# Performance work log

Hardware: AMD Instinct MI355X
Metric: run time of the kernel (lower is better)

The kernel has to match this reference:

```python
import jax, jax.numpy as jnp
import numpy as np

DIM = 1024
DEPTH = 7
PAR = 8
N_NODES = 2 ** (DEPTH + 1) - 1  # 255
WIDTH = PAR * N_NODES  # 2040


def setup_inputs() -> dict:
    key = jax.random.key(0)
    k1, k2, k3, k4 = jax.random.split(key, 4)
    init_k = float(np.sqrt(1.0 / DIM))
    init_k2 = float(np.sqrt(1.0 / ((DEPTH + 1) * PAR)))
    oldx = jax.random.normal(k1, (4, 2048, DIM), dtype=jnp.float32)
    W_in = jax.random.uniform(k2, (WIDTH, DIM), jnp.float32, -init_k, init_k)
    b_in = jax.random.uniform(k3, (WIDTH,), jnp.float32, -init_k, init_k)
    W_out = jax.random.uniform(k4, (DIM, WIDTH), jnp.float32, -init_k2, init_k2)
    return {"oldx": oldx, "W_in": W_in, "b_in": b_in, "W_out": W_out}


def reference(oldx, W_in, b_in, W_out):
    x = oldx.reshape(-1, DIM)                      # [B, dim]
    B = x.shape[0]
    logits = x @ W_in.T + b_in                     # [B, width] dense GEMM over ALL nodes
    decisions = (logits > 0).astype(jnp.int32).reshape(B, PAR, N_NODES)
    acts = jax.nn.silu(logits).reshape(B, PAR, N_NODES)

    # Tree traversal: mark root, then descend DEPTH levels by each node's sign bit.
    current = jnp.zeros((B, PAR), dtype=jnp.int32)
    dmap = jax.nn.one_hot(current, N_NODES, dtype=acts.dtype)  # root node marked
    for d in range(DEPTH):
        cur_platform = 2 ** d - 1
        next_platform = 2 ** (d + 1) - 1
        moves = jnp.take_along_axis(decisions, current[..., None], axis=2)[..., 0]
        current = (current - cur_platform) * 2 + moves + next_platform
        dmap = dmap + jax.nn.one_hot(current, N_NODES, dtype=acts.dtype)

    masked = acts * jax.lax.stop_gradient(dmap)    # only depth+1 nodes per tree survive
    out = masked.reshape(B, WIDTH) @ W_out.T       # [B, dim]
    return out.reshape(oldx.shape)
```

## Files before the change

kernel.cpp:

```cpp
#include <hip/hip_runtime.h>
#include <math.h>

#define DIM 1024
#define DEPTH 7
#define PAR 8
#define N_NODES 255
#define WIDTH 2040
#define MARGIN 0.01f

#define REPLANE(p) ((((p) & 1) << 3) | ((((p) >> 1) & 1) << 4) | ((((p) >> 2) & 1) << 5))

#define PIN4(u) asm volatile("" : "+v"((u).x), "+v"((u).y), "+v"((u).z), "+v"((u).w))

typedef _Float16 half2v __attribute__((ext_vector_type(2)));

__device__ __forceinline__ half2v as_h2(unsigned int u) {
    union { unsigned int u; half2v h; } c; c.u = u; return c.h;
}
__device__ __forceinline__ unsigned int pack_h2(float a, float b) {
    union { half2v h; unsigned int u; } c;
    c.h = (half2v){(_Float16)a, (_Float16)b};
    return c.u;
}

__device__ __forceinline__ float dot2h(unsigned int a, unsigned int b, float c) {
#if __has_builtin(__builtin_amdgcn_fdot2)
    return __builtin_amdgcn_fdot2(as_h2(a), as_h2(b), c, false);
#else
    half2v ha = as_h2(a), hb = as_h2(b);
    c = fmaf((float)ha.x, (float)hb.x, c);
    return fmaf((float)ha.y, (float)hb.y, c);
#endif
}

__device__ __forceinline__ float foldK(float a, float b, int K) {
    const bool hi = (threadIdx.x & (unsigned)K) != 0;
    const float keep = hi ? b : a;
    const float send = hi ? a : b;
    return keep + __shfl_xor(send, K, 64);
}

#define TRANS_BLOCKS 512

__global__ __launch_bounds__(256) void prep_kernel(
    const float* __restrict__ W_out,
    const float* __restrict__ W_in,
    unsigned short* __restrict__ WoT,
    unsigned int* __restrict__ Wh)
{
    __shared__ float tile[64][65];
    if (blockIdx.x < TRANS_BLOCKS) {
        const int w0 = (int)(blockIdx.x & 31) * 64;
        const int d0 = (int)(blockIdx.x >> 5) * 64;
        const int tid = (int)threadIdx.x;
        const int sub = tid & 15;
        const int grp = tid >> 4;

        #pragma unroll
        for (int pass = 0; pass < 4; ++pass) {
            const int dl = pass * 16 + grp;
            const int wl = sub * 4;
            const int w = w0 + wl;
            const int d = d0 + dl;
            float4 v = make_float4(0.f, 0.f, 0.f, 0.f);
            if (w + 3 < WIDTH) {
                v = *(const float4*)(W_out + (size_t)d * WIDTH + w);
            } else {
                float t0 = (w + 0 < WIDTH) ? W_out[(size_t)d * WIDTH + w + 0] : 0.f;
                float t1 = (w + 1 < WIDTH) ? W_out[(size_t)d * WIDTH + w + 1] : 0.f;
                float t2 = (w + 2 < WIDTH) ? W_out[(size_t)d * WIDTH + w + 2] : 0.f;
                float t3 = (w + 3 < WIDTH) ? W_out[(size_t)d * WIDTH + w + 3] : 0.f;
                v = make_float4(t0, t1, t2, t3);
            }
            tile[dl][wl + 0] = v.x; tile[dl][wl + 1] = v.y;
            tile[dl][wl + 2] = v.z; tile[dl][wl + 3] = v.w;
        }
        __syncthreads();
        #pragma unroll
        for (int pass = 0; pass < 4; ++pass) {
            const int wl = pass * 16 + grp;
            const int dl = sub * 4;
            const int w = w0 + wl;
            if (w < WIDTH) {
                uint2 pk;
                pk.x = pack_h2(tile[dl + 0][wl], tile[dl + 1][wl]);
                pk.y = pack_h2(tile[dl + 2][wl], tile[dl + 3][wl]);
                *(uint2*)(WoT + (size_t)w * DIM + d0 + dl) = pk;
            }
        }
    } else {
        const int n4 = WIDTH * DIM / 4;
        const int nthr = ((int)gridDim.x - TRANS_BLOCKS) * 256;
        for (int i = ((int)blockIdx.x - TRANS_BLOCKS) * 256 + (int)threadIdx.x;
             i < n4; i += nthr) {
            float4 v = ((const float4*)W_in)[i];
            uint2 pk;
            pk.x = pack_h2(v.x, v.y);
            pk.y = pack_h2(v.z, v.w);
            ((uint2*)Wh)[i] = pk;
        }
    }
}

__global__ __launch_bounds__(256) void fff_f16_kernel(
    const float* __restrict__ x,
    const float* __restrict__ W_in,
    const float* __restrict__ b_in,
    const unsigned int* __restrict__ Wh,
    const unsigned short* __restrict__ WoT,
    float* __restrict__ out,
    int B)
{
    const int wave = (int)((blockIdx.x * blockDim.x + threadIdx.x) >> 6);
    const int lane = (int)(threadIdx.x & 63);
    if (wave >= B) return;

    const float* xr = x + (size_t)wave * DIM;
    unsigned int xp[8];
    {
        float4 a0 = *(const float4*)(xr + lane * 8 + 0);
        float4 a1 = *(const float4*)(xr + lane * 8 + 4);
        float4 a2 = *(const float4*)(xr + 512 + lane * 8 + 0);
        float4 a3 = *(const float4*)(xr + 512 + lane * 8 + 4);
        xp[0] = pack_h2(a0.x, a0.y);
        xp[1] = pack_h2(a0.z, a0.w);
        xp[2] = pack_h2(a1.x, a1.y);
        xp[3] = pack_h2(a1.z, a1.w);
        xp[4] = pack_h2(a2.x, a2.y);
        xp[5] = pack_h2(a2.z, a2.w);
        xp[6] = pack_h2(a3.x, a3.y);
        xp[7] = pack_h2(a3.z, a3.w);
    }

    float acc[16];
    #pragma unroll
    for (int i = 0; i < 16; ++i) acc[i] = 0.f;

    unsigned long long nodes = 0ULL;
    const int myp = ((lane >> 3) & 1) | (((lane >> 4) & 1) << 1) | (((lane >> 5) & 1) << 2);

    #pragma unroll 1
    for (int d = 0; d <= DEPTH; ++d) {
        int gidx[PAR];
        #pragma unroll
        for (int p = 0; p < PAR; ++p) {
            const int np = (int)((nodes >> (8 * p)) & 0xffULL);
            gidx[p] = p * N_NODES + np;
        }

        const int ga = (lane & 8) ? gidx[1] : gidx[0];
        const int gb = (lane & 8) ? gidx[3] : gidx[2];
        const int gc = (lane & 8) ? gidx[5] : gidx[4];
        const int gd = (lane & 8) ? gidx[7] : gidx[6];
        const int ge = (lane & 16) ? gb : ga;
        const int gf = (lane & 16) ? gd : gc;
        const int gmine = (lane & 32) ? gf : ge;
        const float bias = b_in[gmine];

        uint4 wv0[PAR], wv1[PAR];
        #pragma unroll
        for (int p = 0; p < PAR; ++p) {
            const unsigned short* wo = WoT + (size_t)gidx[p] * DIM;
            wv0[p] = *(const uint4*)(wo + lane * 8);
            wv1[p] = *(const uint4*)(wo + 512 + lane * 8);
        }
        __builtin_amdgcn_sched_barrier(0);

        float partial[PAR];
        #pragma unroll
        for (int p = 0; p < PAR; ++p) {
            const unsigned int* wr = Wh + (size_t)gidx[p] * (DIM / 2);
            const uint4 u0 = *(const uint4*)(wr + lane * 4);
            const uint4 u1 = *(const uint4*)(wr + 256 + lane * 4);
            float s = 0.f;
            s = dot2h(xp[0], u0.x, s);
            s = dot2h(xp[1], u0.y, s);
            s = dot2h(xp[2], u0.z, s);
            s = dot2h(xp[3], u0.w, s);
            s = dot2h(xp[4], u1.x, s);
            s = dot2h(xp[5], u1.y, s);
            s = dot2h(xp[6], u1.z, s);
            s = dot2h(xp[7], u1.w, s);
            partial[p] = s;
        }

        const float c01 = foldK(partial[0], partial[1], 8);
        const float c23 = foldK(partial[2], partial[3], 8);
        const float c45 = foldK(partial[4], partial[5], 8);
        const float c67 = foldK(partial[6], partial[7], 8);
        const float d0f = foldK(c01, c23, 16);
        const float d1f = foldK(c45, c67, 16);
        float e = foldK(d0f, d1f, 32);
        e += __shfl_xor(e, 1, 64);
        e += __shfl_xor(e, 2, 64);
        e += __shfl_xor(e, 4, 64);
        float my = e + bias;

        if (d < DEPTH) {
            const unsigned long long bal = __ballot(fabsf(my) < MARGIN);
            unsigned rm = 0;
            #pragma unroll
            for (int p = 0; p < PAR; ++p)
                rm |= ((unsigned)((bal >> REPLANE(p)) & 1ULL)) << p;
            if (rm) {
                while (rm) {
                    const int p = __builtin_ctz(rm); rm &= (rm - 1u);
                    const int np = (int)((nodes >> (8 * p)) & 0xffULL);
                    const int gi = p * N_NODES + np;
                    const float* wr = W_in + (size_t)gi * DIM;
                    float s = 0.f;
                    #pragma unroll
                    for (int q = 0; q < 4; ++q) {
                        const int off = (q & 1) * 4 + (q >> 1) * 512 + lane * 8;
                        const float4 fx = *(const float4*)(xr + off);
                        const float4 fw = *(const float4*)(wr + off);
                        s = fmaf(fx.x, fw.x, s); s = fmaf(fx.y, fw.y, s);
                        s = fmaf(fx.z, fw.z, s); s = fmaf(fx.w, fw.w, s);
                    }
                    #pragma unroll
                    for (int off = 32; off >= 1; off >>= 1)
                        s += __shfl_xor(s, off, 64);
                    const float lf = s + b_in[gi];
                    my = (myp == p) ? lf : my;
                }
            }
        }

        const float act_mine = my / (1.0f + __expf(-my));
        const unsigned long long pos = __ballot(my > 0.0f);

        float act[PAR];
        #pragma unroll
        for (int p = 0; p < PAR; ++p)
            act[p] = __shfl(act_mine, REPLANE(p), 64);

        #pragma unroll
        for (int p = 0; p < PAR; ++p) { PIN4(wv0[p]); PIN4(wv1[p]); }

        #pragma unroll
        for (int p = 0; p < PAR; ++p) {
            const float a_ = act[p];
            half2v h_;
            h_ = as_h2(wv0[p].x); acc[0]  = fmaf((float)h_.x, a_, acc[0]);  acc[1]  = fmaf((float)h_.y, a_, acc[1]);
            h_ = as_h2(wv0[p].y); acc[2]  = fmaf((float)h_.x, a_, acc[2]);  acc[3]  = fmaf((float)h_.y, a_, acc[3]);
            h_ = as_h2(wv0[p].z); acc[4]  = fmaf((float)h_.x, a_, acc[4]);  acc[5]  = fmaf((float)h_.y, a_, acc[5]);
            h_ = as_h2(wv0[p].w); acc[6]  = fmaf((float)h_.x, a_, acc[6]);  acc[7]  = fmaf((float)h_.y, a_, acc[7]);
            h_ = as_h2(wv1[p].x); acc[8]  = fmaf((float)h_.x, a_, acc[8]);  acc[9]  = fmaf((float)h_.y, a_, acc[9]);
            h_ = as_h2(wv1[p].y); acc[10] = fmaf((float)h_.x, a_, acc[10]); acc[11] = fmaf((float)h_.y, a_, acc[11]);
            h_ = as_h2(wv1[p].z); acc[12] = fmaf((float)h_.x, a_, acc[12]); acc[13] = fmaf((float)h_.y, a_, acc[13]);
            h_ = as_h2(wv1[p].w); acc[14] = fmaf((float)h_.x, a_, acc[14]); acc[15] = fmaf((float)h_.y, a_, acc[15]);
        }

        if (d < DEPTH) {
            #pragma unroll
            for (int p = 0; p < PAR; ++p) {
                const int np = (int)((nodes >> (8 * p)) & 0xffULL);
                const unsigned long long nn = (unsigned long long)
                    (2 * np + 1 + (int)((pos >> REPLANE(p)) & 1ULL));
                nodes = (nodes & ~(0xffULL << (8 * p))) | (nn << (8 * p));
            }
        }
    }

    float* orow = out + (size_t)wave * DIM;
    *(float4*)(orow + lane * 8 + 0)       = make_float4(acc[0],  acc[1],  acc[2],  acc[3]);
    *(float4*)(orow + lane * 8 + 4)       = make_float4(acc[4],  acc[5],  acc[6],  acc[7]);
    *(float4*)(orow + 512 + lane * 8 + 0) = make_float4(acc[8],  acc[9],  acc[10], acc[11]);
    *(float4*)(orow + 512 + lane * 8 + 4) = make_float4(acc[12], acc[13], acc[14], acc[15]);
}

__global__ __launch_bounds__(256) void fff_fallback_kernel(
    const float* __restrict__ x, const float* __restrict__ W_in,
    const float* __restrict__ b_in, const float* __restrict__ W_out,
    float* __restrict__ out, int B)
{
    const int wave = (int)((blockIdx.x * blockDim.x + threadIdx.x) >> 6);
    const int lane = (int)(threadIdx.x & 63);
    if (wave >= B) return;

    const float* xr = x + (size_t)wave * DIM;
    float4 x4[4];
    x4[0] = *(const float4*)(xr + lane * 8 + 0);
    x4[1] = *(const float4*)(xr + lane * 8 + 4);
    x4[2] = *(const float4*)(xr + 512 + lane * 8 + 0);
    x4[3] = *(const float4*)(xr + 512 + lane * 8 + 4);

    float acc[16];
    #pragma unroll
    for (int i = 0; i < 16; ++i) acc[i] = 0.f;
    int node[PAR];
    #pragma unroll
    for (int p = 0; p < PAR; ++p) node[p] = 0;

    for (int d = 0; d <= DEPTH; ++d) {
        #pragma unroll
        for (int p = 0; p < PAR; ++p) {
            const int gidx = p * N_NODES + node[p];
            const float* wr = W_in + (size_t)gidx * DIM;
            const float4 wa = *(const float4*)(wr + lane * 8 + 0);
            const float4 wb = *(const float4*)(wr + lane * 8 + 4);
            const float4 wc = *(const float4*)(wr + 512 + lane * 8 + 0);
            const float4 wd = *(const float4*)(wr + 512 + lane * 8 + 4);
            float s = 0.f;
            s = fmaf(x4[0].x, wa.x, s); s = fmaf(x4[0].y, wa.y, s);
            s = fmaf(x4[0].z, wa.z, s); s = fmaf(x4[0].w, wa.w, s);
            s = fmaf(x4[1].x, wb.x, s); s = fmaf(x4[1].y, wb.y, s);
            s = fmaf(x4[1].z, wb.z, s); s = fmaf(x4[1].w, wb.w, s);
            s = fmaf(x4[2].x, wc.x, s); s = fmaf(x4[2].y, wc.y, s);
            s = fmaf(x4[2].z, wc.z, s); s = fmaf(x4[2].w, wc.w, s);
            s = fmaf(x4[3].x, wd.x, s); s = fmaf(x4[3].y, wd.y, s);
            s = fmaf(x4[3].z, wd.z, s); s = fmaf(x4[3].w, wd.w, s);
            #pragma unroll
            for (int off = 32; off >= 1; off >>= 1)
                s += __shfl_xor(s, off, 64);
            const float logit = s + b_in[gidx];
            const float act = logit / (1.0f + __expf(-logit));
            #pragma unroll
            for (int k = 0; k < 2; ++k) {
                #pragma unroll
                for (int j = 0; j < 8; ++j) {
                    const int e = k * 512 + lane * 8 + j;
                    acc[k * 8 + j] = fmaf(act, W_out[(size_t)e * WIDTH + gidx], acc[k * 8 + j]);
                }
            }
            node[p] = 2 * node[p] + 1 + ((logit > 0.0f) ? 1 : 0);
        }
    }

    float* orow = out + (size_t)wave * DIM;
    *(float4*)(orow + lane * 8 + 0)       = make_float4(acc[0],  acc[1],  acc[2],  acc[3]);
    *(float4*)(orow + lane * 8 + 4)       = make_float4(acc[4],  acc[5],  acc[6],  acc[7]);
    *(float4*)(orow + 512 + lane * 8 + 0) = make_float4(acc[8],  acc[9],  acc[10], acc[11]);
    *(float4*)(orow + 512 + lane * 8 + 4) = make_float4(acc[12], acc[13], acc[14], acc[15]);
}

extern "C" void kernel_launch(void* const* d_in, const int* in_sizes, int n_in,
                              void* d_out, int out_size, void* d_ws, size_t ws_size,
                              hipStream_t stream) {
    const float* oldx  = (const float*)d_in[0];
    const float* W_in  = (const float*)d_in[1];
    const float* b_in  = (const float*)d_in[2];
    const float* W_out = (const float*)d_in[3];
    float* out = (float*)d_out;

    const int B = in_sizes[0] / DIM;

    const size_t half = (size_t)WIDTH * DIM * sizeof(unsigned short);
    const bool use_lp = (ws_size >= 2 * half) && (d_ws != nullptr);

    const int blocks = (B + 3) / 4;

    if (use_lp) {
        unsigned short* WoT = (unsigned short*)d_ws;
        unsigned int*   Wh  = (unsigned int*)((char*)d_ws + half);
        prep_kernel<<<TRANS_BLOCKS + 1024, 256, 0, stream>>>(W_out, W_in, WoT, Wh);
        fff_f16_kernel<<<blocks, 256, 0, stream>>>(oldx, W_in, b_in, Wh, WoT, out, B);
    } else {
        fff_fallback_kernel<<<blocks, 256, 0, stream>>>(oldx, W_in, b_in, W_out, out, B);
    }
}
```

Baseline: 187.1 us.

## Split tree traversal and output accumulation into two kernels via workspace

Splits the fused kernel in two. Stage 1 does the tree traversal and writes per-row activations and node indices to workspace. Stage 2 gathers the fp16 W_out rows and accumulates the output, so each kernel has lower register pressure and stage 1 no longer keeps 16 prefetched W_out vectors live. The cost is an extra kernel launch, a global round trip for the activations and indices, and losing the overlap of W_out loads with the traversal. The split path is used when the workspace is large enough; otherwise the original fused kernel, now without prefetch, runs.

```diff
diff --git a/kernel.cpp b/kernel.cpp
--- a/kernel.cpp
+++ b/kernel.cpp
@@ -9,8 +9,6 @@
 #define MARGIN 0.01f
 
 #define REPLANE(p) ((((p) & 1) << 3) | ((((p) >> 1) & 1) << 4) | ((((p) >> 2) & 1) << 5))
-
-#define PIN4(u) asm volatile("" : "+v"((u).x), "+v"((u).y), "+v"((u).z), "+v"((u).w))
 
 typedef _Float16 half2v __attribute__((ext_vector_type(2)));
 
@@ -102,13 +100,13 @@
     }
 }
 
-__global__ __launch_bounds__(256) void fff_f16_kernel(
+__global__ __launch_bounds__(256) void fff_stage1_kernel(
     const float* __restrict__ x,
     const float* __restrict__ W_in,
     const float* __restrict__ b_in,
     const unsigned int* __restrict__ Wh,
-    const unsigned short* __restrict__ WoT,
-    float* __restrict__ out,
+    float* __restrict__ acts,
+    unsigned short* __restrict__ gidx_out,
     int B)
 {
     const int wave = (int)((blockIdx.x * blockDim.x + threadIdx.x) >> 6);
@@ -132,10 +130,6 @@
         xp[7] = pack_h2(a3.z, a3.w);
     }
 
-    float acc[16];
-    #pragma unroll
-    for (int i = 0; i < 16; ++i) acc[i] = 0.f;
-
     unsigned long long nodes = 0ULL;
     const int myp = ((lane >> 3) & 1) | (((lane >> 4) & 1) << 1) | (((lane >> 5) & 1) << 2);
 
@@ -156,15 +150,6 @@
         const int gf = (lane & 16) ? gd : gc;
         const int gmine = (lane & 32) ? gf : ge;
         const float bias = b_in[gmine];
-
-        uint4 wv0[PAR], wv1[PAR];
-        #pragma unroll
-        for (int p = 0; p < PAR; ++p) {
-            const unsigned short* wo = WoT + (size_t)gidx[p] * DIM;
-            wv0[p] = *(const uint4*)(wo + lane * 8);
-            wv1[p] = *(const uint4*)(wo + 512 + lane * 8);
-        }
-        __builtin_amdgcn_sched_barrier(0);
 
         float partial[PAR];
         #pragma unroll
@@ -229,31 +214,208 @@
         const float act_mine = my / (1.0f + __expf(-my));
         const unsigned long long pos = __ballot(my > 0.0f);
 
-        float act[PAR];
-        #pragma unroll
-        for (int p = 0; p < PAR; ++p)
-            act[p] = __shfl(act_mine, REPLANE(p), 64);
-
-        #pragma unroll
-        for (int p = 0; p < PAR; ++p) { PIN4(wv0[p]); PIN4(wv1[p]); }
-
-        #pragma unroll
-        for (int p = 0; p < PAR; ++p) {
-            const float a_ = act[p];
-            half2v h_;
-            h_ = as_h2(wv0[p].x); acc[0]  = fmaf((float)h_.x, a_, acc[0]);  acc[1]  = fmaf((float)h_.y, a_, acc[1]);
-            h_ = as_h2(wv0[p].y); acc[2]  = fmaf((float)h_.x, a_, acc[2]);  acc[3]  = fmaf((float)h_.y, a_, acc[3]);
-            h_ = as_h2(wv0[p].z); acc[4]  = fmaf((float)h_.x, a_, acc[4]);  acc[5]  = fmaf((float)h_.y, a_, acc[5]);
-            h_ = as_h2(wv0[p].w); acc[6]  = fmaf((float)h_.x, a_, acc[6]);  acc[7]  = fmaf((float)h_.y, a_, acc[7]);
-            h_ = as_h2(wv1[p].x); acc[8]  = fmaf((float)h_.x, a_, acc[8]);  acc[9]  = fmaf((float)h_.y, a_, acc[9]);
-            h_ = as_h2(wv1[p].y); acc[10] = fmaf((float)h_.x, a_, acc[10]); acc[11] = fmaf((float)h_.y, a_, acc[11]);
-            h_ = as_h2(wv1[p].z); acc[12] = fmaf((float)h_.x, a_, acc[12]); acc[13] = fmaf((float)h_.y, a_, acc[13]);
-            h_ = as_h2(wv1[p].w); acc[14] = fmaf((float)h_.x, a_, acc[14]); acc[15] = fmaf((float)h_.y, a_, acc[15]);
+        if ((lane & 7) == 0) {
+            const int slot = (wave << 6) + (d << 3) + myp;
+            acts[slot] = act_mine;
+            gidx_out[slot] = (unsigned short)gmine;
         }
 
         if (d < DEPTH) {
             #pragma unroll
             for (int p = 0; p < PAR; ++p) {
+                const int np = (int)((nodes >> (8 * p)) & 0xffULL);
+                const unsigned long long nn = (unsigned long long)
+                    (2 * np + 1 + (int)((pos >> REPLANE(p)) & 1ULL));
+                nodes = (nodes & ~(0xffULL << (8 * p))) | (nn << (8 * p));
+            }
+        }
+    }
+}
+
+__global__ __launch_bounds__(256) void fff_stage2_kernel(
+    const float* __restrict__ acts,
+    const unsigned short* __restrict__ gidx16,
+    const unsigned short* __restrict__ WoT,
+    float* __restrict__ out,
+    int B)
+{
+    const int wave = (int)((blockIdx.x * blockDim.x + threadIdx.x) >> 6);
+    const int lane = (int)(threadIdx.x & 63);
+    if (wave >= B) return;
+
+    const int base = wave << 6;
+    const float a_l = acts[base + lane];
+    const int   g_l = (int)gidx16[base + lane];
+
+    float acc[16];
+    #pragma unroll
+    for (int i = 0; i < 16; ++i) acc[i] = 0.f;
+
+    #pragma unroll 4
+    for (int e = 0; e < 64; ++e) {
+        const float a_ = __shfl(a_l, e, 64);
+        const int   g  = __shfl(g_l, e, 64);
+        const unsigned short* wo = WoT + (size_t)g * DIM;
+        const uint4 u0 = *(const uint4*)(wo + lane * 8);
+        const uint4 u1 = *(const uint4*)(wo + 512 + lane * 8);
+        half2v h_;
+        h_ = as_h2(u0.x); acc[0]  = fmaf((float)h_.x, a_, acc[0]);  acc[1]  = fmaf((float)h_.y, a_, acc[1]);
+        h_ = as_h2(u0.y); acc[2]  = fmaf((float)h_.x, a_, acc[2]);  acc[3]  = fmaf((float)h_.y, a_, acc[3]);
+        h_ = as_h2(u0.z); acc[4]  = fmaf((float)h_.x, a_, acc[4]);  acc[5]  = fmaf((float)h_.y, a_, acc[5]);
+        h_ = as_h2(u0.w); acc[6]  = fmaf((float)h_.x, a_, acc[6]);  acc[7]  = fmaf((float)h_.y, a_, acc[7]);
+        h_ = as_h2(u1.x); acc[8]  = fmaf((float)h_.x, a_, acc[8]);  acc[9]  = fmaf((float)h_.y, a_, acc[9]);
+        h_ = as_h2(u1.y); acc[10] = fmaf((float)h_.x, a_, acc[10]); acc[11] = fmaf((float)h_.y, a_, acc[11]);
+        h_ = as_h2(u1.z); acc[12] = fmaf((float)h_.x, a_, acc[12]); acc[13] = fmaf((float)h_.y, a_, acc[13]);
+        h_ = as_h2(u1.w); acc[14] = fmaf((float)h_.x, a_, acc[14]); acc[15] = fmaf((float)h_.y, a_, acc[15]);
+    }
+
+    float* orow = out + (size_t)wave * DIM;
+    *(float4*)(orow + lane * 8 + 0)       = make_float4(acc[0],  acc[1],  acc[2],  acc[3]);
+    *(float4*)(orow + lane * 8 + 4)       = make_float4(acc[4],  acc[5],  acc[6],  acc[7]);
+    *(float4*)(orow + 512 + lane * 8 + 0) = make_float4(acc[8],  acc[9],  acc[10], acc[11]);
+    *(float4*)(orow + 512 + lane * 8 + 4) = make_float4(acc[12], acc[13], acc[14], acc[15]);
+}
+
+__global__ __launch_bounds__(256) void fff_f16_kernel(
+    const float* __restrict__ x,
+    const float* __restrict__ W_in,
+    const float* __restrict__ b_in,
+    const unsigned int* __restrict__ Wh,
+    const unsigned short* __restrict__ WoT,
+    float* __restrict__ out,
+    int B)
+{
+    const int wave = (int)((blockIdx.x * blockDim.x + threadIdx.x) >> 6);
+    const int lane = (int)(threadIdx.x & 63);
+    if (wave >= B) return;
+
+    const float* xr = x + (size_t)wave * DIM;
+    unsigned int xp[8];
+    {
+        float4 a0 = *(const float4*)(xr + lane * 8 + 0);
+        float4 a1 = *(const float4*)(xr + lane * 8 + 4);
+        float4 a2 = *(const float4*)(xr + 512 + lane * 8 + 0);
+        float4 a3 = *(const float4*)(xr + 512 + lane * 8 + 4);
+        xp[0] = pack_h2(a0.x, a0.y);
+        xp[1] = pack_h2(a0.z, a0.w);
+        xp[2] = pack_h2(a1.x, a1.y);
+        xp[3] = pack_h2(a1.z, a1.w);
+        xp[4] = pack_h2(a2.x, a2.y);
+        xp[5] = pack_h2(a2.z, a2.w);
+        xp[6] = pack_h2(a3.x, a3.y);
+        xp[7] = pack_h2(a3.z, a3.w);
+    }
+
+    float acc[16];
+    #pragma unroll
+    for (int i = 0; i < 16; ++i) acc[i] = 0.f;
+
+    unsigned long long nodes = 0ULL;
+    const int myp = ((lane >> 3) & 1) | (((lane >> 4) & 1) << 1) | (((lane >> 5) & 1) << 2);
+
+    #pragma unroll 1
+    for (int d = 0; d <= DEPTH; ++d) {
+        int gidx[PAR];
+        #pragma unroll
+        for (int p = 0; p < PAR; ++p) {
+            const int np = (int)((nodes >> (8 * p)) & 0xffULL);
+            gidx[p] = p * N_NODES + np;
+        }
+
+        const int ga = (lane & 8) ? gidx[1] : gidx[0];
+        const int gb = (lane & 8) ? gidx[3] : gidx[2];
+        const int gc = (lane & 8) ? gidx[5] : gidx[4];
+        const int gd = (lane & 8) ? gidx[7] : gidx[6];
+        const int ge = (lane & 16) ? gb : ga;
+        const int gf = (lane & 16) ? gd : gc;
+        const int gmine = (lane & 32) ? gf : ge;
+        const float bias = b_in[gmine];
+
+        float partial[PAR];
+        #pragma unroll
+        for (int p = 0; p < PAR; ++p) {
+            const unsigned int* wr = Wh + (size_t)gidx[p] * (DIM / 2);
+            const uint4 u0 = *(const uint4*)(wr + lane * 4);
+            const uint4 u1 = *(const uint4*)(wr + 256 + lane * 4);
+            float s = 0.f;
+            s = dot2h(xp[0], u0.x, s);
+            s = dot2h(xp[1], u0.y, s);
+            s = dot2h(xp[2], u0.z, s);
+            s = dot2h(xp[3], u0.w, s);
+            s = dot2h(xp[4], u1.x, s);
+            s = dot2h(xp[5], u1.y, s);
+            s = dot2h(xp[6], u1.z, s);
+            s = dot2h(xp[7], u1.w, s);
+            partial[p] = s;
+        }
+
+        const float c01 = foldK(partial[0], partial[1], 8);
+        const float c23 = foldK(partial[2], partial[3], 8);
+        const float c45 = foldK(partial[4], partial[5], 8);
+        const float c67 = foldK(partial[6], partial[7], 8);
+        const float d0f = foldK(c01, c23, 16);
+        const float d1f = foldK(c45, c67, 16);
+        float e = foldK(d0f, d1f, 32);
+        e += __shfl_xor(e, 1, 64);
+        e += __shfl_xor(e, 2, 64);
+        e += __shfl_xor(e, 4, 64);
+        float my = e + bias;
+
+        if (d < DEPTH) {
+            const unsigned long long bal = __ballot(fabsf(my) < MARGIN);
+            unsigned rm = 0;
+            #pragma unroll
+            for (int p = 0; p < PAR; ++p)
+                rm |= ((unsigned)((bal >> REPLANE(p)) & 1ULL)) << p;
+            if (rm) {
+                while (rm) {
+                    const int p = __builtin_ctz(rm); rm &= (rm - 1u);
+                    const int np = (int)((nodes >> (8 * p)) & 0xffULL);
+                    const int gi = p * N_NODES + np;
+                    const float* wr = W_in + (size_t)gi * DIM;
+                    float s = 0.f;
+                    #pragma unroll
+                    for (int q = 0; q < 4; ++q) {
+                        const int off = (q & 1) * 4 + (q >> 1) * 512 + lane * 8;
+                        const float4 fx = *(const float4*)(xr + off);
+                        const float4 fw = *(const float4*)(wr + off);
+                        s = fmaf(fx.x, fw.x, s); s = fmaf(fx.y, fw.y, s);
+                        s = fmaf(fx.z, fw.z, s); s = fmaf(fx.w, fw.w, s);
+                    }
+                    #pragma unroll
+                    for (int off = 32; off >= 1; off >>= 1)
+                        s += __shfl_xor(s, off, 64);
+                    const float lf = s + b_in[gi];
+                    my = (myp == p) ? lf : my;
+                }
+            }
+        }
+
+        const float act_mine = my / (1.0f + __expf(-my));
+        const unsigned long long pos = __ballot(my > 0.0f);
+
+        float act[PAR];
+        #pragma unroll
+        for (int p = 0; p < PAR; ++p)
+            act[p] = __shfl(act_mine, REPLANE(p), 64);
+
+        #pragma unroll
+        for (int p = 0; p < PAR; ++p) {
+            const unsigned short* wo = WoT + (size_t)gidx[p] * DIM;
+            const uint4 u0 = *(const uint4*)(wo + lane * 8);
+            const uint4 u1 = *(const uint4*)(wo + 512 + lane * 8);
+            const float a_ = act[p];
+            half2v h_;
+            h_ = as_h2(u0.x); acc[0]  = fmaf((float)h_.x, a_, acc[0]);  acc[1]  = fmaf((float)h_.y, a_, acc[1]);
+            h_ = as_h2(u0.y); acc[2]  = fmaf((float)h_.x, a_, acc[2]);  acc[3]  = fmaf((float)h_.y, a_, acc[3]);
+            h_ = as_h2(u0.z); acc[4]  = fmaf((float)h_.x, a_, acc[4]);  acc[5]  = fmaf((float)h_.y, a_, acc[5]);
+            h_ = as_h2(u0.w); acc[6]  = fmaf((float)h_.x, a_, acc[6]);  acc[7]  = fmaf((float)h_.y, a_, acc[7]);
+            h_ = as_h2(u1.x); acc[8]  = fmaf((float)h_.x, a_, acc[8]);  acc[9]  = fmaf((float)h_.y, a_, acc[9]);
+            h_ = as_h2(u1.y); acc[10] = fmaf((float)h_.x, a_, acc[10]); acc[11] = fmaf((float)h_.y, a_, acc[11]);
+            h_ = as_h2(u1.z); acc[12] = fmaf((float)h_.x, a_, acc[12]); acc[13] = fmaf((float)h_.y, a_, acc[13]);
+            h_ = as_h2(u1.w); acc[14] = fmaf((float)h_.x, a_, acc[14]); acc[15] = fmaf((float)h_.y, a_, acc[15]);
+
+            if (d < DEPTH) {
                 const int np = (int)((nodes >> (8 * p)) & 0xffULL);
                 const unsigned long long nn = (unsigned long long)
                     (2 * np + 1 + (int)((pos >> REPLANE(p)) & 1ULL));
@@ -345,12 +507,23 @@
 
     const int B = in_sizes[0] / DIM;
 
-    const size_t half = (size_t)WIDTH * DIM * sizeof(unsigned short);
-    const bool use_lp = (ws_size >= 2 * half) && (d_ws != nullptr);
+    const size_t half   = (size_t)WIDTH * DIM * sizeof(unsigned short);
+    const size_t actsz  = (size_t)B * 64 * sizeof(float);
+    const size_t idxsz  = (size_t)B * 64 * sizeof(unsigned short);
+    const bool use_split = (d_ws != nullptr) && (ws_size >= 2 * half + actsz + idxsz);
+    const bool use_lp    = (d_ws != nullptr) && (ws_size >= 2 * half);
 
     const int blocks = (B + 3) / 4;
 
-    if (use_lp) {
+    if (use_split) {
+        unsigned short* WoT  = (unsigned short*)d_ws;
+        unsigned int*   Wh   = (unsigned int*)((char*)d_ws + half);
+        float*          acts = (float*)((char*)d_ws + 2 * half);
+        unsigned short* gidx = (unsigned short*)((char*)d_ws + 2 * half + actsz);
+        prep_kernel<<<TRANS_BLOCKS + 1024, 256, 0, stream>>>(W_out, W_in, WoT, Wh);
+        fff_stage1_kernel<<<blocks, 256, 0, stream>>>(oldx, W_in, b_in, Wh, acts, gidx, B);
+        fff_stage2_kernel<<<blocks, 256, 0, stream>>>(acts, gidx, WoT, out, B);
+    } else if (use_lp) {
         unsigned short* WoT = (unsigned short*)d_ws;
         unsigned int*   Wh  = (unsigned int*)((char*)d_ws + half);
         prep_kernel<<<TRANS_BLOCKS + 1024, 256, 0, stream>>>(W_out, W_in, WoT, Wh);
```

Measured after the change: 181.1 us. 3.2% less time.
